# Kernel optimization log

Measured on AMD Instinct MI355X. Metric: run time of the kernel, lower is better.

## Reference

```python
import jax, jax.numpy as jnp
import numpy as np

N, F_IN, D_OUT, H = 8192, 512, 64, 8
ALPHA = 0.2
NEG_INF = jnp.float32(-9e15)


def setup_inputs() -> dict:
    key = jax.random.key(0)
    k1, k2, k3, k4, k5 = jax.random.split(key, 5)
    x = jax.random.normal(k1, (N, F_IN), dtype=jnp.float32)
    # sparse-ish binary adjacency (avg degree ~33) with self-loops, stored dense
    adj = (jax.random.uniform(k2, (N, N)) < 0.004).astype(jnp.float32)
    adj = jnp.maximum(adj, jnp.eye(N, dtype=jnp.float32))
    W = jax.random.normal(k3, (H, F_IN, D_OUT), dtype=jnp.float32) * 0.05
    a1 = jax.random.normal(k4, (H, D_OUT), dtype=jnp.float32) * 0.05
    a2 = jax.random.normal(k5, (H, D_OUT), dtype=jnp.float32) * 0.05
    return {"x": x, "adj": adj, "W": W, "a1": a1, "a2": a2}


def reference(x, adj, W, a1, a2):
    mask = adj > 0
    outputs = []
    for h in range(H):  # fixed small head count (matches original per-head loop)
        Wh = x @ W[h]                      # [N, D]
        f1 = Wh @ a1[h]                    # [N]
        f2 = Wh @ a2[h]                    # [N]
        e = jax.nn.leaky_relu(f1[:, None] + f2[None, :], ALPHA)  # [N, N]
        att = jnp.where(mask, e, NEG_INF)
        att = jax.nn.softmax(att, axis=1)  # dropout omitted (eval mode)
        outputs.append(att @ Wh)           # [N, D]
    return jnp.concatenate(outputs, axis=1)  # [N, H*D]
```

## Files before the change

kernel.cpp:

```cpp
#include <hip/hip_runtime.h>
#include <hip/hip_bf16.h>
#include <cstdint>

#define N_NODES 8192
#define F_IN    512
#define D_O     64
#define H_N     8
#define NOUT    512
#define MAXD    128

#define BM 64
#define BN 128
#define BK 64

typedef __attribute__((ext_vector_type(8))) short short8;
typedef __attribute__((ext_vector_type(4))) float f32x4;

static __device__ __forceinline__ ushort f2bf(float f) {
  union { float f; uint32_t u; } v; v.f = f;
  uint32_t r = v.u + 0x7FFFu + ((v.u >> 16) & 1u);
  return (ushort)(r >> 16);
}
static __device__ __forceinline__ float bf2f(ushort u) {
  union { uint32_t u; float f; } v; v.u = ((uint32_t)u) << 16;
  return v.f;
}

__global__ __launch_bounds__(256) void convert(const float* __restrict__ x,
                                               const float* __restrict__ W,
                                               ushort* __restrict__ xb,
                                               ushort* __restrict__ Wt) {
  __shared__ float Ws[64][65];
  const int b = blockIdx.x, t = threadIdx.x;
  if (b < 2048) {
    const int gid = b * 256 + t;
    #pragma unroll
    for (int it = 0; it < 2; ++it) {
      const int q = gid + it * 524288;
      const float4 v = ((const float4*)x)[q];
      ushort4 u;
      u.x = f2bf(v.x); u.y = f2bf(v.y); u.z = f2bf(v.z); u.w = f2bf(v.w);
      ((ushort4*)xb)[q] = u;
    }
  } else {
    const int bb = b - 2048;
    const int h = bb >> 3, kt = bb & 7;
    const int d = t & 63, krg = (t >> 6) * 16;
    const float* src = &W[((size_t)h * F_IN + kt * 64 + krg) * D_O + d];
    #pragma unroll
    for (int q = 0; q < 16; ++q)
      Ws[krg + q][d] = src[(size_t)q * D_O];
    __syncthreads();
    const int d0 = t >> 2, kq = (t & 3) * 16;
    ushort* dst = &Wt[(size_t)h * D_O * F_IN + (size_t)d0 * F_IN + kt * 64 + kq];
    #pragma unroll
    for (int q = 0; q < 16; ++q)
      dst[q] = f2bf(Ws[kq + q][d0]);
  }
}

__global__ __launch_bounds__(256) void scan_gemm(const uint32_t* __restrict__ adj,
                                                 const ushort* __restrict__ xb,
                                                 const ushort* __restrict__ Wt,
                                                 const float* __restrict__ a1,
                                                 const float* __restrict__ a2,
                                                 ushort* __restrict__ Whb,
                                                 float* __restrict__ f1,
                                                 float* __restrict__ f2,
                                                 int* __restrict__ nbr_g,
                                                 int* __restrict__ deg_g) {
  __shared__ ushort As[BM][BK + 8];
  __shared__ ushort Bs[BN][BK + 8];
  __shared__ int wsum[4];

  const int id   = blockIdx.x;
  const int tid  = threadIdx.x;
  const int lane = tid & 63;
  const int wv   = tid >> 6;

  if (id < 512) {
    const int wr = wv >> 1, wc = wv & 1;
    const int r0 = (id >> 2) * BM;
    const int c0 = (id & 3) * BN;
    const int lm = lane & 15;
    const int lg = lane >> 4;

    f32x4 acc[2][4];
    #pragma unroll
    for (int m2 = 0; m2 < 2; ++m2)
      #pragma unroll
      for (int n2 = 0; n2 < 4; ++n2)
        acc[m2][n2] = (f32x4){0.f, 0.f, 0.f, 0.f};

    for (int k0 = 0; k0 < F_IN; k0 += BK) {
      __syncthreads();
      #pragma unroll
      for (int p = 0; p < 2; ++p) {
        const int e = p * 256 + tid;
        const int row = e >> 3, ck = (e & 7) * 8;
        *(short8*)&As[row][ck] = *(const short8*)&xb[(size_t)(r0 + row) * F_IN + k0 + ck];
      }
      #pragma unroll
      for (int p = 0; p < 4; ++p) {
        const int e = p * 256 + tid;
        const int row = e >> 3, ck = (e & 7) * 8;
        *(short8*)&Bs[row][ck] = *(const short8*)&Wt[(size_t)(c0 + row) * F_IN + k0 + ck];
      }
      __syncthreads();

      #pragma unroll
      for (int kk = 0; kk < 2; ++kk) {
        const int koff = kk * 32 + lg * 8;
        short8 af[2], bf[4];
        #pragma unroll
        for (int m2 = 0; m2 < 2; ++m2)
          af[m2] = *(const short8*)&As[wr * 32 + m2 * 16 + lm][koff];
        #pragma unroll
        for (int n2 = 0; n2 < 4; ++n2)
          bf[n2] = *(const short8*)&Bs[wc * 64 + n2 * 16 + lm][koff];
        #pragma unroll
        for (int m2 = 0; m2 < 2; ++m2)
          #pragma unroll
          for (int n2 = 0; n2 < 4; ++n2)
            acc[m2][n2] = __builtin_amdgcn_mfma_f32_16x16x32_bf16(af[m2], bf[n2], acc[m2][n2], 0, 0, 0);
      }
    }

    const int head = (c0 >> 6) + wc;
    float a1v[4], a2v[4];
    #pragma unroll
    for (int n2 = 0; n2 < 4; ++n2) {
      a1v[n2] = a1[head * D_O + n2 * 16 + lm];
      a2v[n2] = a2[head * D_O + n2 * 16 + lm];
    }
    #pragma unroll
    for (int m2 = 0; m2 < 2; ++m2) {
      #pragma unroll
      for (int r = 0; r < 4; ++r) {
        const int row = r0 + wr * 32 + m2 * 16 + lg * 4 + r;
        float p1 = 0.f, p2 = 0.f;
        #pragma unroll
        for (int n2 = 0; n2 < 4; ++n2) {
          const float v = acc[m2][n2][r];
          p1 += v * a1v[n2];
          p2 += v * a2v[n2];
          Whb[(size_t)row * NOUT + c0 + wc * 64 + n2 * 16 + lm] = f2bf(v);
        }
        #pragma unroll
        for (int o = 1; o < 16; o <<= 1) {
          p1 += __shfl_xor(p1, o);
          p2 += __shfl_xor(p2, o);
        }
        if (lm == 0) {
          f1[(size_t)row * H_N + head] = p1;
          f2[(size_t)row * H_N + head] = p2;
        }
      }
    }
  } else {
    const int i = id - 512;
    const uint32_t* arow = adj + (size_t)i * N_NODES;
    uint32_t bits = 0;
    #pragma unroll
    for (int u = 0; u < 8; ++u) {
      const uint4 a = *(const uint4*)&arow[(u * 256 + tid) * 4];
      if (a.x) bits |= 1u << (u * 4 + 0);
      if (a.y) bits |= 1u << (u * 4 + 1);
      if (a.z) bits |= 1u << (u * 4 + 2);
      if (a.w) bits |= 1u << (u * 4 + 3);
    }
    const int cnt = __popc(bits);
    int v = cnt;
    #pragma unroll
    for (int o = 1; o < 64; o <<= 1) {
      int u = __shfl_up(v, o);
      if (lane >= o) v += u;
    }
    if (lane == 63) wsum[wv] = v;
    __syncthreads();
    int base = 0, total = 0;
    #pragma unroll
    for (int ww = 0; ww < 4; ++ww) {
      int s = wsum[ww];
      if (ww < wv) base += s;
      total += s;
    }
    int off = base + v - cnt;
    #pragma unroll
    for (int u = 0; u < 8; ++u)
      #pragma unroll
      for (int bq = 0; bq < 4; ++bq)
        if (bits & (1u << (u * 4 + bq))) {
          if (off < MAXD) nbr_g[(size_t)i * MAXD + off] = (u * 256 + tid) * 4 + bq;
          ++off;
        }
    if (tid == 0) deg_g[i] = min(total, MAXD);
  }
}

__global__ __launch_bounds__(128) void gat_attn(const int* __restrict__ nbr_g,
                                                const int* __restrict__ deg_g,
                                                const ushort* __restrict__ Whb,
                                                const float* __restrict__ f1,
                                                const float* __restrict__ f2,
                                                float* __restrict__ out) {
  const int i    = blockIdx.x;
  const int tid  = threadIdx.x;
  const int lane = tid & 63;
  const int w    = tid >> 6;

  __shared__ int   nbr[MAXD];
  __shared__ float p[MAXD][9];
  __shared__ float f1s[8], invs[8];

  const int deg = deg_g[i];
  if (tid < 8) f1s[tid] = f1[(size_t)i * H_N + tid];
  nbr[tid] = nbr_g[(size_t)i * MAXD + tid];
  __syncthreads();

  for (int idx = tid; idx < deg * H_N; idx += 128) {
    const int n = idx >> 3, h = idx & 7;
    const int j = nbr[n];
    float l = f1s[h] + f2[(size_t)j * H_N + h];
    l = l > 0.f ? l : 0.2f * l;
    p[n][h] = l;
  }
  __syncthreads();

  #pragma unroll
  for (int hh = 0; hh < 4; ++hh) {
    const int h = w * 4 + hh;
    float m = -3.0e38f;
    for (int n = lane; n < deg; n += 64) m = fmaxf(m, p[n][h]);
    #pragma unroll
    for (int o = 32; o; o >>= 1) m = fmaxf(m, __shfl_xor(m, o));
    float s = 0.f;
    for (int n = lane; n < deg; n += 64) {
      const float e = __expf(p[n][h] - m);
      p[n][h] = e;
      s += e;
    }
    #pragma unroll
    for (int o = 32; o; o >>= 1) s += __shfl_xor(s, o);
    if (lane == 0) invs[h] = 1.0f / s;
  }
  __syncthreads();

  const int h = tid >> 4;
  float a0 = 0.f, a1c = 0.f, a2c = 0.f, a3 = 0.f;
  #pragma unroll 8
  for (int n = 0; n < deg; ++n) {
    const float pv = p[n][h];
    const ushort4 u = *(const ushort4*)&Whb[(size_t)nbr[n] * NOUT + tid * 4];
    a0  += pv * bf2f(u.x);
    a1c += pv * bf2f(u.y);
    a2c += pv * bf2f(u.z);
    a3  += pv * bf2f(u.w);
  }
  const float inv = invs[h];
  float4 o4;
  o4.x = a0 * inv; o4.y = a1c * inv; o4.z = a2c * inv; o4.w = a3 * inv;
  *(float4*)&out[(size_t)i * NOUT + tid * 4] = o4;
}

extern "C" void kernel_launch(void* const* d_in, const int* in_sizes, int n_in,
                              void* d_out, int out_size, void* d_ws, size_t ws_size,
                              hipStream_t stream) {
  const float* x   = (const float*)d_in[0];
  const float* adj = (const float*)d_in[1];
  const float* W   = (const float*)d_in[2];
  const float* a1  = (const float*)d_in[3];
  const float* a2  = (const float*)d_in[4];
  float* out = (float*)d_out;

  ushort* Whb = (ushort*)d_ws;
  ushort* xb  = Whb + (size_t)N_NODES * NOUT;
  ushort* Wt  = xb + (size_t)N_NODES * F_IN;
  float*  f1  = (float*)(Wt + (size_t)H_N * D_O * F_IN);
  float*  f2  = f1 + (size_t)N_NODES * H_N;
  int*    nbr_g = (int*)(f2 + (size_t)N_NODES * H_N);
  int*    deg_g = nbr_g + (size_t)N_NODES * MAXD;

  hipLaunchKernelGGL(convert, dim3(2112), dim3(256), 0, stream, x, W, xb, Wt);
  hipLaunchKernelGGL(scan_gemm, dim3(512 + N_NODES), dim3(256), 0, stream,
                     (const uint32_t*)adj, xb, Wt, a1, a2, Whb, f1, f2, nbr_g, deg_g);
  hipLaunchKernelGGL(gat_attn, dim3(N_NODES), dim3(128), 0, stream,
                     nbr_g, deg_g, Whb, f1, f2, out);
}
```

Measured before the change: 102.6 us.

## Split attention kernel into four head-pair panels per node with single-wave blocks

Replaces the per-node 128-thread attention block with four 64-thread blocks per node, each handling two heads (a 128-column panel). Each block loads only its two f2 values per neighbour, fuses the leaky-relu into the max pass, and gathers ushort2 per thread instead of ushort4. The aim is more, smaller blocks for better occupancy and latency hiding in the gather. In exchange, the neighbour list and degree are reloaded four times per node and each gather access is narrower.

```diff
diff --git a/kernel.cpp b/kernel.cpp
--- a/kernel.cpp
+++ b/kernel.cpp
@@ -198,69 +198,72 @@
   }
 }
 
-__global__ __launch_bounds__(128) void gat_attn(const int* __restrict__ nbr_g,
+__global__ __launch_bounds__(64) void gat_panel(const int* __restrict__ nbr_g,
                                                 const int* __restrict__ deg_g,
                                                 const ushort* __restrict__ Whb,
                                                 const float* __restrict__ f1,
                                                 const float* __restrict__ f2,
                                                 float* __restrict__ out) {
-  const int i    = blockIdx.x;
-  const int tid  = threadIdx.x;
-  const int lane = tid & 63;
-  const int w    = tid >> 6;
+  const int bid = blockIdx.x;
+  const int P   = bid >> 13;
+  const int i   = bid & 8191;
+  const int t   = threadIdx.x;
 
   __shared__ int   nbr[MAXD];
-  __shared__ float p[MAXD][9];
-  __shared__ float f1s[8], invs[8];
+  __shared__ float ff[MAXD][2];
+  __shared__ float ps[MAXD][2];
+  __shared__ float f1s2[2], invs2[2];
 
   const int deg = deg_g[i];
-  if (tid < 8) f1s[tid] = f1[(size_t)i * H_N + tid];
-  nbr[tid] = nbr_g[(size_t)i * MAXD + tid];
+  if (t < deg)      nbr[t]      = nbr_g[(size_t)i * MAXD + t];
+  if (t + 64 < deg) nbr[t + 64] = nbr_g[(size_t)i * MAXD + t + 64];
+  if (t < 2) f1s2[t] = f1[(size_t)i * H_N + 2 * P + t];
   __syncthreads();
 
-  for (int idx = tid; idx < deg * H_N; idx += 128) {
-    const int n = idx >> 3, h = idx & 7;
-    const int j = nbr[n];
-    float l = f1s[h] + f2[(size_t)j * H_N + h];
-    l = l > 0.f ? l : 0.2f * l;
-    p[n][h] = l;
+  for (int n = t; n < deg; n += 64) {
+    const float2 v = *(const float2*)&f2[(size_t)nbr[n] * H_N + 2 * P];
+    ff[n][0] = v.x; ff[n][1] = v.y;
   }
   __syncthreads();
 
-  #pragma unroll
-  for (int hh = 0; hh < 4; ++hh) {
-    const int h = w * 4 + hh;
+  {
+    const int h = t >> 5;
+    const int l = t & 31;
+    const float f1v = f1s2[h];
     float m = -3.0e38f;
-    for (int n = lane; n < deg; n += 64) m = fmaxf(m, p[n][h]);
-    #pragma unroll
-    for (int o = 32; o; o >>= 1) m = fmaxf(m, __shfl_xor(m, o));
+    for (int n = l; n < deg; n += 32) {
+      float e = f1v + ff[n][h];
+      e = e > 0.f ? e : 0.2f * e;
+      ps[n][h] = e;
+      m = fmaxf(m, e);
+    }
+    #pragma unroll
+    for (int o = 16; o; o >>= 1) m = fmaxf(m, __shfl_xor(m, o));
     float s = 0.f;
-    for (int n = lane; n < deg; n += 64) {
-      const float e = __expf(p[n][h] - m);
-      p[n][h] = e;
+    for (int n = l; n < deg; n += 32) {
+      const float e = __expf(ps[n][h] - m);
+      ps[n][h] = e;
       s += e;
     }
     #pragma unroll
-    for (int o = 32; o; o >>= 1) s += __shfl_xor(s, o);
-    if (lane == 0) invs[h] = 1.0f / s;
+    for (int o = 16; o; o >>= 1) s += __shfl_xor(s, o);
+    if (l == 0) invs2[h] = 1.0f / s;
   }
   __syncthreads();
 
-  const int h = tid >> 4;
-  float a0 = 0.f, a1c = 0.f, a2c = 0.f, a3 = 0.f;
+  const int ht      = t >> 5;
+  const int colbase = P * 128 + t * 2;
+  float a0 = 0.f, a1c = 0.f;
   #pragma unroll 8
   for (int n = 0; n < deg; ++n) {
-    const float pv = p[n][h];
-    const ushort4 u = *(const ushort4*)&Whb[(size_t)nbr[n] * NOUT + tid * 4];
+    const float pv = ps[n][ht];
+    const ushort2 u = *(const ushort2*)&Whb[(size_t)nbr[n] * NOUT + colbase];
     a0  += pv * bf2f(u.x);
     a1c += pv * bf2f(u.y);
-    a2c += pv * bf2f(u.z);
-    a3  += pv * bf2f(u.w);
-  }
-  const float inv = invs[h];
-  float4 o4;
-  o4.x = a0 * inv; o4.y = a1c * inv; o4.z = a2c * inv; o4.w = a3 * inv;
-  *(float4*)&out[(size_t)i * NOUT + tid * 4] = o4;
+  }
+  const float inv = invs2[ht];
+  float2 o2; o2.x = a0 * inv; o2.y = a1c * inv;
+  *(float2*)&out[(size_t)i * NOUT + colbase] = o2;
 }
 
 extern "C" void kernel_launch(void* const* d_in, const int* in_sizes, int n_in,
@@ -284,6 +287,6 @@
   hipLaunchKernelGGL(convert, dim3(2112), dim3(256), 0, stream, x, W, xb, Wt);
   hipLaunchKernelGGL(scan_gemm, dim3(512 + N_NODES), dim3(256), 0, stream,
                      (const uint32_t*)adj, xb, Wt, a1, a2, Whb, f1, f2, nbr_g, deg_g);
-  hipLaunchKernelGGL(gat_attn, dim3(N_NODES), dim3(128), 0, stream,
+  hipLaunchKernelGGL(gat_panel, dim3(4 * N_NODES), dim3(64), 0, stream,
                      nbr_g, deg_g, Whb, f1, f2, out);
 }
```

New measurement: 94.06 us. 1.09x faster.
